# Performance work log

Measured on AMD Instinct MI355X. Metric: run time of the kernel, lower is better.

## Reference

```python
import jax, jax.numpy as jnp
from jax import lax
import numpy as np

T, B, NIN = 512, 512, 64
H1, H2, H3 = 100, 50, 25


def lstm_layer(x, w_ih, w_hh, b_ih, b_hh):
    # x: [T, B, in]; torch gate order (i, f, g, o); weights [4H, in]/[4H, H]
    H = w_hh.shape[1]
    xg = jnp.einsum('tbi,gi->tbg', x, w_ih) + b_ih + b_hh  # [T, B, 4H]

    def step(carry, xg_t):
        h, c = carry
        g = xg_t + h @ w_hh.T
        i, f, gg, o = jnp.split(g, 4, axis=-1)
        c = jax.nn.sigmoid(f) * c + jax.nn.sigmoid(i) * jnp.tanh(gg)
        h = jax.nn.sigmoid(o) * jnp.tanh(c)
        return (h, c), h

    h0 = jnp.zeros((x.shape[1], H), x.dtype)
    _, hs = lax.scan(step, (h0, h0), xg)
    return hs  # [T, B, H]


def setup_inputs() -> dict:
    key = jax.random.key(0)
    ks = jax.random.split(key, 16)
    s = 0.1  # init scale for stability
    return {
        'x': jax.random.normal(ks[0], (T, B, NIN), jnp.float32),
        'w_ih1': jax.random.normal(ks[1], (4 * H1, NIN), jnp.float32) * s,
        'w_hh1': jax.random.normal(ks[2], (4 * H1, H1), jnp.float32) * s,
        'b_ih1': jax.random.normal(ks[3], (4 * H1,), jnp.float32) * s,
        'b_hh1': jax.random.normal(ks[4], (4 * H1,), jnp.float32) * s,
        'w_ih2': jax.random.normal(ks[5], (4 * H2, H1), jnp.float32) * s,
        'w_hh2': jax.random.normal(ks[6], (4 * H2, H2), jnp.float32) * s,
        'b_ih2': jax.random.normal(ks[7], (4 * H2,), jnp.float32) * s,
        'b_hh2': jax.random.normal(ks[8], (4 * H2,), jnp.float32) * s,
        'w_ih3': jax.random.normal(ks[9], (4 * H3, H2), jnp.float32) * s,
        'w_hh3': jax.random.normal(ks[10], (4 * H3, H3), jnp.float32) * s,
        'b_ih3': jax.random.normal(ks[11], (4 * H3,), jnp.float32) * s,
        'b_hh3': jax.random.normal(ks[12], (4 * H3,), jnp.float32) * s,
        'w_lin': jax.random.normal(ks[13], (1, H3), jnp.float32) * s,
        'b_lin': jax.random.normal(ks[14], (1,), jnp.float32) * s,
    }


def reference(x, w_ih1, w_hh1, b_ih1, b_hh1,
              w_ih2, w_hh2, b_ih2, b_hh2,
              w_ih3, w_hh3, b_ih3, b_hh3,
              w_lin, b_lin):
    # Dropout layers are identity at inference.
    h = lstm_layer(x, w_ih1, w_hh1, b_ih1, b_hh1)
    h = lstm_layer(h, w_ih2, w_hh2, b_ih2, b_hh2)
    h = lstm_layer(h, w_ih3, w_hh3, b_ih3, b_hh3)
    return h @ w_lin.T + b_lin  # [T, B, 1]
```

## Files before the change

### kernel.cpp

```cpp
#include <hip/hip_runtime.h>
#include <math.h>

#define T_STEPS 512
#define BATCH   512

__device__ __forceinline__ float sigmoidf_(float x) {
    return 1.0f / (1.0f + __expf(-x));
}
__device__ __forceinline__ float tanhf_(float x) {
    float ax = fabsf(x);
    float e  = __expf(-2.0f * ax);
    float t  = (1.0f - e) / (1.0f + e);
    return copysignf(t, x);
}
__device__ __forceinline__ float4 ld4(const float* p) {
    return make_float4(p[0], p[1], p[2], p[3]);
}

__global__ __launch_bounds__(448, 2) void gemm1_kernel(
    const float* __restrict__ A, const float* __restrict__ W,
    const float* __restrict__ bih, const float* __restrict__ bhh,
    float* __restrict__ xg)
{
    __shared__ __align__(16) float As[64 * 64];
    const int tid = threadIdx.x;

    float4 W00,W01,W02,W03,W04,W05,W06,W07,W08,W09,W10,W11,W12,W13,W14,W15;
    float bias = 0.0f;
    if (tid < 400) {
        bias = bih[tid] + bhh[tid];
        const float* wp = W + tid * 64;
        W00=ld4(wp+ 0); W01=ld4(wp+ 4); W02=ld4(wp+ 8); W03=ld4(wp+12);
        W04=ld4(wp+16); W05=ld4(wp+20); W06=ld4(wp+24); W07=ld4(wp+28);
        W08=ld4(wp+32); W09=ld4(wp+36); W10=ld4(wp+40); W11=ld4(wp+44);
        W12=ld4(wp+48); W13=ld4(wp+52); W14=ld4(wp+56); W15=ld4(wp+60);
    }

    const size_t r0 = (size_t)blockIdx.x * 64;
    const float4* Ag = (const float4*)(A + r0 * 64);
    float4* As4 = (float4*)As;
    for (int i = tid; i < 64 * 16; i += 448) As4[i] = Ag[i];
    __syncthreads();

    if (tid < 400) {
        for (int r = 0; r < 64; ++r) {
            const float4* a4 = (const float4*)(As + r * 64);
            float a0 = bias, a1 = 0.0f;
#define G1V(WV, I) { float4 v = a4[I]; \
            a0 = fmaf(v.x, WV.x, a0); a1 = fmaf(v.y, WV.y, a1); \
            a0 = fmaf(v.z, WV.z, a0); a1 = fmaf(v.w, WV.w, a1); }
            G1V(W00,0) G1V(W01,1) G1V(W02,2) G1V(W03,3)
            G1V(W04,4) G1V(W05,5) G1V(W06,6) G1V(W07,7)
            G1V(W08,8) G1V(W09,9) G1V(W10,10) G1V(W11,11)
            G1V(W12,12) G1V(W13,13) G1V(W14,14) G1V(W15,15)
#undef G1V
            xg[(r0 + r) * 400 + tid] = a0 + a1;
        }
    }
}

__global__ __launch_bounds__(448, 2) void gemm2_kernel(
    const float* __restrict__ A,
    const float* __restrict__ W,
    const float* __restrict__ bih, const float* __restrict__ bhh,
    float* __restrict__ xg)
{
    __shared__ __align__(16) float As[64 * 104];
    __shared__ __align__(16) float ps[8][2][200];

    const int tid  = threadIdx.x;
    const bool slot = (tid < 400);
    const int q = slot ? tid / 200 : 0;
    const int j = slot ? tid % 200 : 0;

    float4 W00,W01,W02,W03,W04,W05,W06,W07,W08,W09,W10,W11,W12;
    float bias = 0.0f;
    if (slot) {
        if (q == 0) bias = bih[j] + bhh[j];
        const float* wp = W + j * 100 + q * 52;
        W00=ld4(wp+ 0); W01=ld4(wp+ 4); W02=ld4(wp+ 8); W03=ld4(wp+12);
        W04=ld4(wp+16); W05=ld4(wp+20); W06=ld4(wp+24); W07=ld4(wp+28);
        W08=ld4(wp+32); W09=ld4(wp+36); W10=ld4(wp+40); W11=ld4(wp+44);
        W12 = q ? make_float4(0.f,0.f,0.f,0.f) : ld4(wp+48);
    }

    const size_t r0 = (size_t)blockIdx.x * 64;
    const float2* A2 = (const float2*)(A + r0 * 100);
    float2* As2 = (float2*)As;
    for (int i = tid; i < 64 * 50; i += 448) {
        int r = i / 50, k2 = i % 50;
        As2[r * 52 + k2] = A2[i];
    }
    if (tid < 64) {
        As[tid*104+100]=0.f; As[tid*104+101]=0.f;
        As[tid*104+102]=0.f; As[tid*104+103]=0.f;
    }
    __syncthreads();

    const float4* As4 = (const float4*)As;
    const int q13 = q * 13;
    const float base = (q == 0) ? bias : 0.0f;
    for (int g = 0; g < 8; ++g) {
        const int rb = g * 8;
        if (slot) {
#define G2V(P, WV, I) { float4 v = P[I]; \
            A0 = fmaf(v.x, WV.x, A0); A1 = fmaf(v.y, WV.y, A1); \
            A0 = fmaf(v.z, WV.z, A0); A1 = fmaf(v.w, WV.w, A1); }
#define G2ROW(RR) { const float4* a4 = As4 + (rb + RR) * 26 + q13; \
            float A0 = base, A1 = 0.0f; \
            G2V(a4,W00,0) G2V(a4,W01,1) G2V(a4,W02,2) G2V(a4,W03,3) \
            G2V(a4,W04,4) G2V(a4,W05,5) G2V(a4,W06,6) G2V(a4,W07,7) \
            G2V(a4,W08,8) G2V(a4,W09,9) G2V(a4,W10,10) G2V(a4,W11,11) \
            G2V(a4,W12,12) \
            ps[RR][q][j] = A0 + A1; }
            G2ROW(0) G2ROW(1) G2ROW(2) G2ROW(3)
            G2ROW(4) G2ROW(5) G2ROW(6) G2ROW(7)
#undef G2ROW
#undef G2V
        }
        __syncthreads();
        if (tid < 200) {
            #pragma unroll
            for (int rr = 0; rr < 8; ++rr)
                xg[(r0 + rb + rr) * 200 + tid] = ps[rr][0][tid] + ps[rr][1][tid];
        }
        __syncthreads();
    }
}

__global__ __launch_bounds__(832, 3) void scan1_kernel(
    const float* __restrict__ xg,
    const float* __restrict__ w_hh,
    float* __restrict__ h1c,
    float* __restrict__ c1state,
    int t0, int CH)
{
    __shared__ __align__(16) float h_s[2][104];
    __shared__ __align__(16) float ps[2][2][400];

    const int tid   = threadIdx.x;
    const int q     = (tid >= 416) ? 1 : 0;
    const int j     = tid - 416 * q;
    const bool slot = (j < 400);
    const int brow0 = blockIdx.x * 2;

    float4 W00,W01,W02,W03,W04,W05,W06,W07,W08,W09,W10,W11,W12;
    if (slot) {
        const float* wp = w_hh + j * 100 + q * 52;
        W00=ld4(wp+ 0); W01=ld4(wp+ 4); W02=ld4(wp+ 8); W03=ld4(wp+12);
        W04=ld4(wp+16); W05=ld4(wp+20); W06=ld4(wp+24); W07=ld4(wp+28);
        W08=ld4(wp+32); W09=ld4(wp+36); W10=ld4(wp+40); W11=ld4(wp+44);
        W12 = q ? make_float4(0.f,0.f,0.f,0.f) : ld4(wp+48);
    }

    float c = 0.0f;
    if (tid < 200) {
        int bn = tid / 100, u = tid % 100;
        if (t0 == 0) {
            h_s[bn][u] = 0.0f;
        } else {
            h_s[bn][u] = h1c[((size_t)(CH - 1) * BATCH + brow0 + bn) * 100 + u];
            c          = c1state[(size_t)(brow0 + bn) * 100 + u];
        }
    }
    if (tid >= 200 && tid < 208) {
        int i = tid - 200;
        h_s[i >> 2][100 + (i & 3)] = 0.0f;
    }

    float xgv0 = 0.0f, xgv1 = 0.0f;
    if (slot && q == 0) {
        xgv0 = xg[(size_t)brow0 * 400 + j];
        xgv1 = xg[((size_t)brow0 + 1) * 400 + j];
    }
    __syncthreads();

    const int hq = q * 13;
    for (int tl = 0; tl < CH; ++tl) {
        float pre0 = 0.0f, pre1 = 0.0f;
        if (slot && q == 0 && tl + 1 < CH) {
            pre0 = xg[((size_t)(tl + 1) * BATCH + brow0) * 400 + j];
            pre1 = xg[((size_t)(tl + 1) * BATCH + brow0 + 1) * 400 + j];
        }
        if (slot) {
            const float4* h0 = (const float4*)h_s[0] + hq;
            const float4* h1 = (const float4*)h_s[1] + hq;
            float a00 = xgv0, a01 = 0.0f, a10 = xgv1, a11 = 0.0f;
#define S1ACC(WV, I) { float4 v0 = h0[I], v1 = h1[I]; \
            a00 = fmaf(v0.x, WV.x, a00); a10 = fmaf(v1.x, WV.x, a10); \
            a01 = fmaf(v0.y, WV.y, a01); a11 = fmaf(v1.y, WV.y, a11); \
            a00 = fmaf(v0.z, WV.z, a00); a10 = fmaf(v1.z, WV.z, a10); \
            a01 = fmaf(v0.w, WV.w, a01); a11 = fmaf(v1.w, WV.w, a11); }
            S1ACC(W00,0) S1ACC(W01,1) S1ACC(W02,2) S1ACC(W03,3)
            S1ACC(W04,4) S1ACC(W05,5) S1ACC(W06,6) S1ACC(W07,7)
            S1ACC(W08,8) S1ACC(W09,9) S1ACC(W10,10) S1ACC(W11,11)
            S1ACC(W12,12)
#undef S1ACC
            ps[0][q][j] = a00 + a01;
            ps[1][q][j] = a10 + a11;
        }
        __syncthreads();
        xgv0 = pre0; xgv1 = pre1;
        if (tid < 200) {
            int bn = tid / 100, u = tid % 100;
            float gi = ps[bn][0][u]       + ps[bn][1][u];
            float gf = ps[bn][0][100 + u] + ps[bn][1][100 + u];
            float gg = ps[bn][0][200 + u] + ps[bn][1][200 + u];
            float go = ps[bn][0][300 + u] + ps[bn][1][300 + u];
            c = sigmoidf_(gf) * c + sigmoidf_(gi) * tanhf_(gg);
            float h = sigmoidf_(go) * tanhf_(c);
            h_s[bn][u] = h;
            h1c[((size_t)tl * BATCH + brow0 + bn) * 100 + u] = h;
        }
        __syncthreads();
    }
    if (tid < 200) {
        int bn = tid / 100, u = tid % 100;
        c1state[(size_t)(brow0 + bn) * 100 + u] = c;
    }
}

__global__ __launch_bounds__(384, 2) void scan23_kernel(
    const float* __restrict__ xg2,
    const float* __restrict__ w_hh2,
    const float* __restrict__ w_ih3,
    const float* __restrict__ w_hh3,
    const float* __restrict__ b_ih3, const float* __restrict__ b_hh3,
    const float* __restrict__ w_lin, const float* __restrict__ b_lin,
    float* __restrict__ out,
    float* __restrict__ h2state, float* __restrict__ c2state,
    float* __restrict__ h3state, float* __restrict__ c3state,
    int t0, int CH)
{
    __shared__ __align__(16) float h2_s[52];
    __shared__ __align__(16) float x3_s[2][52];
    __shared__ __align__(16) float h3_s[28];
    __shared__ __align__(16) float h3o_s[2][28];
    __shared__ __align__(16) float g2_s[200];
    __shared__ __align__(16) float g3_s[100];

    const int tid  = threadIdx.x;
    const int brow = blockIdx.x;

    float4 WA0,WA1,WA2,WA3,WA4,WA5,WA6,WA7,WA8,WA9,WA10,WA11,WA12;
    float4 WB0,WB1,WB2,WB3,WB4,WB5,WB6;
    float bias = 0.0f;

    if (tid < 200) {
        const float* p = w_hh2 + tid * 50;
        WA0=ld4(p+ 0); WA1=ld4(p+ 4); WA2=ld4(p+ 8); WA3=ld4(p+12);
        WA4=ld4(p+16); WA5=ld4(p+20); WA6=ld4(p+24); WA7=ld4(p+28);
        WA8=ld4(p+32); WA9=ld4(p+36); WA10=ld4(p+40); WA11=ld4(p+44);
        WA12 = make_float4(p[48], p[49], 0.f, 0.f);
    } else if (tid >= 256 && tid < 356) {
        int jj = tid - 256;
        bias = b_ih3[jj] + b_hh3[jj];
        const float* p = w_ih3 + jj * 50;
        WA0=ld4(p+ 0); WA1=ld4(p+ 4); WA2=ld4(p+ 8); WA3=ld4(p+12);
        WA4=ld4(p+16); WA5=ld4(p+20); WA6=ld4(p+24); WA7=ld4(p+28);
        WA8=ld4(p+32); WA9=ld4(p+36); WA10=ld4(p+40); WA11=ld4(p+44);
        WA12 = make_float4(p[48], p[49], 0.f, 0.f);
        const float* p2 = w_hh3 + jj * 25;
        WB0=ld4(p2+ 0); WB1=ld4(p2+ 4); WB2=ld4(p2+ 8);
        WB3=ld4(p2+12); WB4=ld4(p2+16); WB5=ld4(p2+20);
        WB6 = make_float4(p2[24], 0.f, 0.f, 0.f);
    } else if (tid == 370) {
        bias = b_lin[0];
        WA0=ld4(w_lin+ 0); WA1=ld4(w_lin+ 4); WA2=ld4(w_lin+ 8);
        WA3=ld4(w_lin+12); WA4=ld4(w_lin+16); WA5=ld4(w_lin+20);
        WA6 = make_float4(w_lin[24], 0.f, 0.f, 0.f);
    }

    float c2 = 0.0f, c3 = 0.0f;
    if (tid < 52)  { h2_s[tid] = 0.0f; x3_s[0][tid] = 0.0f; x3_s[1][tid] = 0.0f; }
    if (tid >= 52 && tid < 80)  h3_s[tid - 52] = 0.0f;
    if (tid >= 80 && tid < 108) h3o_s[0][tid - 80] = 0.0f;
    if (tid >= 108 && tid < 136) h3o_s[1][tid - 108] = 0.0f;
    __syncthreads();
    if (t0 > 0) {
        if (tid < 50) {
            h2_s[tid] = h2state[(size_t)brow * 50 + tid];
            c2        = c2state[(size_t)brow * 50 + tid];
        }
        if (tid >= 256 && tid < 281) {
            int u = tid - 256;
            h3_s[u] = h3state[(size_t)brow * 25 + u];
            c3      = c3state[(size_t)brow * 25 + u];
        }
    }
    float xgv = (tid < 200) ? xg2[(size_t)brow * 200 + tid] : 0.0f;
    __syncthreads();

    for (int it = 0; it < CH + 2; ++it) {
        float pre = (tid < 200 && it + 1 < CH)
                  ? xg2[((size_t)(it + 1) * BATCH + brow) * 200 + tid] : 0.0f;

        if (tid < 200 && it < CH) {
            const float4* hv = (const float4*)h2_s;
            float a0 = xgv, a1 = 0.0f;
#define SCV(PV, WV, I) { float4 v = PV[I]; \
            a0 = fmaf(v.x, WV.x, a0); a1 = fmaf(v.y, WV.y, a1); \
            a0 = fmaf(v.z, WV.z, a0); a1 = fmaf(v.w, WV.w, a1); }
            SCV(hv,WA0,0) SCV(hv,WA1,1) SCV(hv,WA2,2) SCV(hv,WA3,3)
            SCV(hv,WA4,4) SCV(hv,WA5,5) SCV(hv,WA6,6) SCV(hv,WA7,7)
            SCV(hv,WA8,8) SCV(hv,WA9,9) SCV(hv,WA10,10) SCV(hv,WA11,11)
            SCV(hv,WA12,12)
            g2_s[tid] = a0 + a1;
        }

        if (tid >= 256 && tid < 356 && it >= 1 && it <= CH) {
            const float4* xv = (const float4*)x3_s[(it - 1) & 1];
            const float4* hv = (const float4*)h3_s;
            float a0 = bias, a1 = 0.0f;
            SCV(xv,WA0,0) SCV(xv,WA1,1) SCV(xv,WA2,2) SCV(xv,WA3,3)
            SCV(xv,WA4,4) SCV(xv,WA5,5) SCV(xv,WA6,6) SCV(xv,WA7,7)
            SCV(xv,WA8,8) SCV(xv,WA9,9) SCV(xv,WA10,10) SCV(xv,WA11,11)
            SCV(xv,WA12,12)
            SCV(hv,WB0,0) SCV(hv,WB1,1) SCV(hv,WB2,2) SCV(hv,WB3,3)
            SCV(hv,WB4,4) SCV(hv,WB5,5) SCV(hv,WB6,6)
            g3_s[tid - 256] = a0 + a1;
        }

        if (tid == 370 && it >= 2) {
            const float4* hv = (const float4*)h3o_s[(it - 2) & 1];
            float a0 = bias, a1 = 0.0f;
            SCV(hv,WA0,0) SCV(hv,WA1,1) SCV(hv,WA2,2) SCV(hv,WA3,3)
            SCV(hv,WA4,4) SCV(hv,WA5,5) SCV(hv,WA6,6)
            out[(size_t)(t0 + it - 2) * BATCH + brow] = a0 + a1;
        }
#undef SCV
        __syncthreads();

        if (tid < 200) xgv = pre;

        if (tid < 50 && it < CH) {
            float gi = g2_s[tid],       gf = g2_s[50 + tid];
            float gg = g2_s[100 + tid], go = g2_s[150 + tid];
            c2 = sigmoidf_(gf) * c2 + sigmoidf_(gi) * tanhf_(gg);
            float h = sigmoidf_(go) * tanhf_(c2);
            h2_s[tid] = h;
            x3_s[it & 1][tid] = h;
        }

        if (tid >= 256 && tid < 281 && it >= 1 && it <= CH) {
            int u = tid - 256;
            float gi = g3_s[u],      gf = g3_s[25 + u];
            float gg = g3_s[50 + u], go = g3_s[75 + u];
            c3 = sigmoidf_(gf) * c3 + sigmoidf_(gi) * tanhf_(gg);
            float h = sigmoidf_(go) * tanhf_(c3);
            h3_s[u] = h;
            h3o_s[(it - 1) & 1][u] = h;
        }
        __syncthreads();
    }

    if (tid < 50) {
        h2state[(size_t)brow * 50 + tid] = h2_s[tid];
        c2state[(size_t)brow * 50 + tid] = c2;
    }
    if (tid >= 256 && tid < 281) {
        int u = tid - 256;
        h3state[(size_t)brow * 25 + u] = h3_s[u];
        c3state[(size_t)brow * 25 + u] = c3;
    }
}

extern "C" void kernel_launch(void* const* d_in, const int* in_sizes, int n_in,
                              void* d_out, int out_size, void* d_ws, size_t ws_size,
                              hipStream_t stream)
{
    const float* x     = (const float*)d_in[0];
    const float* w_ih1 = (const float*)d_in[1];
    const float* w_hh1 = (const float*)d_in[2];
    const float* b_ih1 = (const float*)d_in[3];
    const float* b_hh1 = (const float*)d_in[4];
    const float* w_ih2 = (const float*)d_in[5];
    const float* w_hh2 = (const float*)d_in[6];
    const float* b_ih2 = (const float*)d_in[7];
    const float* b_hh2 = (const float*)d_in[8];
    const float* w_ih3 = (const float*)d_in[9];
    const float* w_hh3 = (const float*)d_in[10];
    const float* b_ih3 = (const float*)d_in[11];
    const float* b_hh3 = (const float*)d_in[12];
    const float* w_lin = (const float*)d_in[13];
    const float* b_lin = (const float*)d_in[14];
    float* out = (float*)d_out;

    const size_t state_bytes = (size_t)BATCH * (100 + 50 + 50 + 25 + 25) * sizeof(float);
    int CH = 0;
    for (int c = 128; c >= 8; c >>= 1) {
        size_t need = (size_t)c * BATCH * 700 * sizeof(float) + state_bytes;
        if (need <= ws_size) { CH = c; break; }
    }
    if (CH == 0) return;

    char* ws = (char*)d_ws;
    float* xg1c    = (float*)ws;
    float* h1c     = xg1c + (size_t)CH * BATCH * 400;
    float* xg2c    = h1c  + (size_t)CH * BATCH * 100;
    float* c1state = xg2c + (size_t)CH * BATCH * 200;
    float* h2state = c1state + (size_t)BATCH * 100;
    float* c2state = h2state + (size_t)BATCH * 50;
    float* h3state = c2state + (size_t)BATCH * 50;
    float* c3state = h3state + (size_t)BATCH * 25;

    const int rowtiles = CH * BATCH / 64;

    for (int t0 = 0; t0 < T_STEPS; t0 += CH) {
        gemm1_kernel<<<rowtiles, 448, 0, stream>>>(
            x + (size_t)t0 * BATCH * 64, w_ih1, b_ih1, b_hh1, xg1c);
        scan1_kernel<<<BATCH / 2, 832, 0, stream>>>(xg1c, w_hh1, h1c, c1state, t0, CH);
        gemm2_kernel<<<rowtiles, 448, 0, stream>>>(h1c, w_ih2, b_ih2, b_hh2, xg2c);
        scan23_kernel<<<BATCH, 384, 0, stream>>>(
            xg2c, w_hh2, w_ih3, w_hh3, b_ih3, b_hh3, w_lin, b_lin, out,
            h2state, c2state, h3state, c3state, t0, CH);
    }
}
```

Before: 1.909 ms.

## Give each thread all four gates of a hidden unit in LSTM scans

Restructures scan1 and scan23 so each thread computes all four gate pre-activations (i,f,g,o) for one hidden unit, keeping the four weight rows in registers. The nonlinearity can then run on values the thread already holds, without a shared-memory gate exchange. scan1 moves from two batch rows per 832-thread block to one row per 256-thread block. h state is double-buffered so fewer shared-memory round trips sit between the matvec and the cell update. The cost is much higher register pressure (about 52 float4 weights per thread, pinned with inline asm) and fewer active lanes per block, which risks spills or lower occupancy.

Result: slower. 5.776 ms (+202.6%).

```diff
diff --git a/kernel.cpp b/kernel.cpp
--- a/kernel.cpp
+++ b/kernel.cpp
@@ -16,6 +16,9 @@
 __device__ __forceinline__ float4 ld4(const float* p) {
     return make_float4(p[0], p[1], p[2], p[3]);
 }
+
+#define PINF(f)  asm volatile("" : "+v"(f))
+#define PIN4(v)  { PINF(v.x); PINF(v.y); PINF(v.z); PINF(v.w); }
 
 __global__ __launch_bounds__(448, 2) void gemm1_kernel(
     const float* __restrict__ A, const float* __restrict__ W,
@@ -60,8 +63,7 @@
 }
 
 __global__ __launch_bounds__(448, 2) void gemm2_kernel(
-    const float* __restrict__ A,
-    const float* __restrict__ W,
+    const float* __restrict__ A, const float* __restrict__ W,
     const float* __restrict__ bih, const float* __restrict__ bhh,
     float* __restrict__ xg)
 {
@@ -128,7 +130,7 @@
     }
 }
 
-__global__ __launch_bounds__(832, 3) void scan1_kernel(
+__global__ __launch_bounds__(256, 2) void scan1_kernel(
     const float* __restrict__ xg,
     const float* __restrict__ w_hh,
     float* __restrict__ h1c,
@@ -136,91 +138,87 @@
     int t0, int CH)
 {
     __shared__ __align__(16) float h_s[2][104];
-    __shared__ __align__(16) float ps[2][2][400];
-
-    const int tid   = threadIdx.x;
-    const int q     = (tid >= 416) ? 1 : 0;
-    const int j     = tid - 416 * q;
-    const bool slot = (j < 400);
-    const int brow0 = blockIdx.x * 2;
-
-    float4 W00,W01,W02,W03,W04,W05,W06,W07,W08,W09,W10,W11,W12;
-    if (slot) {
-        const float* wp = w_hh + j * 100 + q * 52;
-        W00=ld4(wp+ 0); W01=ld4(wp+ 4); W02=ld4(wp+ 8); W03=ld4(wp+12);
-        W04=ld4(wp+16); W05=ld4(wp+20); W06=ld4(wp+24); W07=ld4(wp+28);
-        W08=ld4(wp+32); W09=ld4(wp+36); W10=ld4(wp+40); W11=ld4(wp+44);
-        W12 = q ? make_float4(0.f,0.f,0.f,0.f) : ld4(wp+48);
-    }
-
+    __shared__ __align__(16) float ps[2][4][100];
+
+    const int tid = threadIdx.x;
+    const int row = blockIdx.x;
+    const bool act = (tid < 200);
+    const int u = act ? tid % 100 : 0;
+    const int q = act ? tid / 100 : 0;
+
+    float4 A0,A1,A2,A3,A4,A5,A6,A7,A8,A9,A10,A11,A12;
+    float4 B0,B1,B2,B3,B4,B5,B6,B7,B8,B9,B10,B11,B12;
+    float4 C0,C1,C2,C3,C4,C5,C6,C7,C8,C9,C10,C11,C12;
+    float4 D0,D1,D2,D3,D4,D5,D6,D7,D8,D9,D10,D11,D12;
+#define S1LD(P, base) \
+    P##0=ld4(base+0);  P##1=ld4(base+4);  P##2=ld4(base+8);  P##3=ld4(base+12); \
+    P##4=ld4(base+16); P##5=ld4(base+20); P##6=ld4(base+24); P##7=ld4(base+28); \
+    P##8=ld4(base+32); P##9=ld4(base+36); P##10=ld4(base+40); P##11=ld4(base+44); \
+    P##12 = q ? make_float4(0.f,0.f,0.f,0.f) : ld4(base+48); \
+    PIN4(P##0) PIN4(P##1) PIN4(P##2) PIN4(P##3) PIN4(P##4) PIN4(P##5) \
+    PIN4(P##6) PIN4(P##7) PIN4(P##8) PIN4(P##9) PIN4(P##10) PIN4(P##11) PIN4(P##12)
+    if (act) {
+        const float* wi = w_hh + (0 * 100 + u) * 100 + q * 52;
+        const float* wf = w_hh + (1 * 100 + u) * 100 + q * 52;
+        const float* wg = w_hh + (2 * 100 + u) * 100 + q * 52;
+        const float* wo = w_hh + (3 * 100 + u) * 100 + q * 52;
+        S1LD(A, wi) S1LD(B, wf) S1LD(C, wg) S1LD(D, wo)
+    }
+#undef S1LD
+
+    if (tid < 208) { int b = tid / 104, i = tid % 104; h_s[b][i] = 0.0f; }
     float c = 0.0f;
-    if (tid < 200) {
-        int bn = tid / 100, u = tid % 100;
-        if (t0 == 0) {
-            h_s[bn][u] = 0.0f;
-        } else {
-            h_s[bn][u] = h1c[((size_t)(CH - 1) * BATCH + brow0 + bn) * 100 + u];
-            c          = c1state[(size_t)(brow0 + bn) * 100 + u];
-        }
-    }
-    if (tid >= 200 && tid < 208) {
-        int i = tid - 200;
-        h_s[i >> 2][100 + (i & 3)] = 0.0f;
-    }
-
-    float xgv0 = 0.0f, xgv1 = 0.0f;
-    if (slot && q == 0) {
-        xgv0 = xg[(size_t)brow0 * 400 + j];
-        xgv1 = xg[((size_t)brow0 + 1) * 400 + j];
-    }
-    __syncthreads();
-
-    const int hq = q * 13;
+    __syncthreads();
+    if (t0 > 0 && tid < 100) {
+        h_s[0][u] = h1c[((size_t)(CH - 1) * BATCH + row) * 100 + u];
+        c         = c1state[(size_t)row * 100 + u];
+    }
+    float xgI = 0.f, xgF = 0.f, xgG = 0.f, xgO = 0.f;
+    if (tid < 100) {
+        const float* xp = xg + (size_t)row * 400 + u;
+        xgI = xp[0]; xgF = xp[100]; xgG = xp[200]; xgO = xp[300];
+    }
+    __syncthreads();
+
     for (int tl = 0; tl < CH; ++tl) {
-        float pre0 = 0.0f, pre1 = 0.0f;
-        if (slot && q == 0 && tl + 1 < CH) {
-            pre0 = xg[((size_t)(tl + 1) * BATCH + brow0) * 400 + j];
-            pre1 = xg[((size_t)(tl + 1) * BATCH + brow0 + 1) * 400 + j];
-        }
-        if (slot) {
-            const float4* h0 = (const float4*)h_s[0] + hq;
-            const float4* h1 = (const float4*)h_s[1] + hq;
-            float a00 = xgv0, a01 = 0.0f, a10 = xgv1, a11 = 0.0f;
-#define S1ACC(WV, I) { float4 v0 = h0[I], v1 = h1[I]; \
-            a00 = fmaf(v0.x, WV.x, a00); a10 = fmaf(v1.x, WV.x, a10); \
-            a01 = fmaf(v0.y, WV.y, a01); a11 = fmaf(v1.y, WV.y, a11); \
-            a00 = fmaf(v0.z, WV.z, a00); a10 = fmaf(v1.z, WV.z, a10); \
-            a01 = fmaf(v0.w, WV.w, a01); a11 = fmaf(v1.w, WV.w, a11); }
-            S1ACC(W00,0) S1ACC(W01,1) S1ACC(W02,2) S1ACC(W03,3)
-            S1ACC(W04,4) S1ACC(W05,5) S1ACC(W06,6) S1ACC(W07,7)
-            S1ACC(W08,8) S1ACC(W09,9) S1ACC(W10,10) S1ACC(W11,11)
-            S1ACC(W12,12)
-#undef S1ACC
-            ps[0][q][j] = a00 + a01;
-            ps[1][q][j] = a10 + a11;
-        }
-        __syncthreads();
-        xgv0 = pre0; xgv1 = pre1;
-        if (tid < 200) {
-            int bn = tid / 100, u = tid % 100;
-            float gi = ps[bn][0][u]       + ps[bn][1][u];
-            float gf = ps[bn][0][100 + u] + ps[bn][1][100 + u];
-            float gg = ps[bn][0][200 + u] + ps[bn][1][200 + u];
-            float go = ps[bn][0][300 + u] + ps[bn][1][300 + u];
+        float pI = 0.f, pF = 0.f, pG = 0.f, pO = 0.f;
+        if (tid < 100 && tl + 1 < CH) {
+            const float* xp = xg + ((size_t)(tl + 1) * BATCH + row) * 400 + u;
+            pI = xp[0]; pF = xp[100]; pG = xp[200]; pO = xp[300];
+        }
+        if (act) {
+            const float4* hv = (const float4*)h_s[tl & 1] + q * 13;
+            float aI = q ? 0.f : xgI, aF = q ? 0.f : xgF;
+            float aG = q ? 0.f : xgG, aO = q ? 0.f : xgO;
+#define S1F(I) { float4 v = hv[I]; \
+            aI=fmaf(v.x,A##I.x,aI); aF=fmaf(v.x,B##I.x,aF); aG=fmaf(v.x,C##I.x,aG); aO=fmaf(v.x,D##I.x,aO); \
+            aI=fmaf(v.y,A##I.y,aI); aF=fmaf(v.y,B##I.y,aF); aG=fmaf(v.y,C##I.y,aG); aO=fmaf(v.y,D##I.y,aO); \
+            aI=fmaf(v.z,A##I.z,aI); aF=fmaf(v.z,B##I.z,aF); aG=fmaf(v.z,C##I.z,aG); aO=fmaf(v.z,D##I.z,aO); \
+            aI=fmaf(v.w,A##I.w,aI); aF=fmaf(v.w,B##I.w,aF); aG=fmaf(v.w,C##I.w,aG); aO=fmaf(v.w,D##I.w,aO); }
+            S1F(0) S1F(1) S1F(2) S1F(3) S1F(4) S1F(5) S1F(6)
+            S1F(7) S1F(8) S1F(9) S1F(10) S1F(11) S1F(12)
+#undef S1F
+            ps[q][0][u] = aI; ps[q][1][u] = aF;
+            ps[q][2][u] = aG; ps[q][3][u] = aO;
+        }
+        __syncthreads();
+        xgI = pI; xgF = pF; xgG = pG; xgO = pO;
+        if (tid < 100) {
+            float gi = ps[0][0][u] + ps[1][0][u];
+            float gf = ps[0][1][u] + ps[1][1][u];
+            float gg = ps[0][2][u] + ps[1][2][u];
+            float go = ps[0][3][u] + ps[1][3][u];
             c = sigmoidf_(gf) * c + sigmoidf_(gi) * tanhf_(gg);
             float h = sigmoidf_(go) * tanhf_(c);
-            h_s[bn][u] = h;
-            h1c[((size_t)tl * BATCH + brow0 + bn) * 100 + u] = h;
-        }
-        __syncthreads();
-    }
-    if (tid < 200) {
-        int bn = tid / 100, u = tid % 100;
-        c1state[(size_t)(brow0 + bn) * 100 + u] = c;
-    }
-}
-
-__global__ __launch_bounds__(384, 2) void scan23_kernel(
+            h_s[(tl + 1) & 1][u] = h;
+            h1c[((size_t)tl * BATCH + row) * 100 + u] = h;
+        }
+        __syncthreads();
+    }
+    if (tid < 100) c1state[(size_t)row * 100 + u] = c;
+}
+
+__global__ __launch_bounds__(128, 2) void scan23_kernel(
     const float* __restrict__ xg2,
     const float* __restrict__ w_hh2,
     const float* __restrict__ w_ih3,
@@ -232,136 +230,164 @@
     float* __restrict__ h3state, float* __restrict__ c3state,
     int t0, int CH)
 {
-    __shared__ __align__(16) float h2_s[52];
+    __shared__ __align__(16) float h2_s[2][52];
     __shared__ __align__(16) float x3_s[2][52];
-    __shared__ __align__(16) float h3_s[28];
+    __shared__ __align__(16) float h3_s[2][28];
     __shared__ __align__(16) float h3o_s[2][28];
-    __shared__ __align__(16) float g2_s[200];
-    __shared__ __align__(16) float g3_s[100];
-
-    const int tid  = threadIdx.x;
-    const int brow = blockIdx.x;
-
+    __shared__ __align__(16) float ps3[2][25];
+
+    const int tid = threadIdx.x;
+    const int row = blockIdx.x;
+
+    const bool isL2 = (tid < 50);
+    const bool isL3 = (tid >= 64 && tid < 114);
+    const bool isLin = (tid == 120);
+    const int u2 = isL2 ? tid : 0;
+    const int u3 = isL3 ? (tid - 64) % 25 : 0;
+    const int p3 = isL3 ? (tid - 64) / 25 : 0;
+
+    float4 A0,A1,A2,A3,A4,A5,A6,A7,A8,A9,A10,A11,A12;
+    float4 B0,B1,B2,B3,B4,B5,B6,B7,B8,B9,B10,B11,B12;
+    float4 C0,C1,C2,C3,C4,C5,C6,C7,C8,C9,C10,C11,C12;
+    float4 D0,D1,D2,D3,D4,D5,D6,D7,D8,D9,D10,D11,D12;
     float4 WA0,WA1,WA2,WA3,WA4,WA5,WA6,WA7,WA8,WA9,WA10,WA11,WA12;
     float4 WB0,WB1,WB2,WB3,WB4,WB5,WB6;
-    float bias = 0.0f;
-
-    if (tid < 200) {
-        const float* p = w_hh2 + tid * 50;
-        WA0=ld4(p+ 0); WA1=ld4(p+ 4); WA2=ld4(p+ 8); WA3=ld4(p+12);
-        WA4=ld4(p+16); WA5=ld4(p+20); WA6=ld4(p+24); WA7=ld4(p+28);
-        WA8=ld4(p+32); WA9=ld4(p+36); WA10=ld4(p+40); WA11=ld4(p+44);
-        WA12 = make_float4(p[48], p[49], 0.f, 0.f);
-    } else if (tid >= 256 && tid < 356) {
-        int jj = tid - 256;
-        bias = b_ih3[jj] + b_hh3[jj];
-        const float* p = w_ih3 + jj * 50;
-        WA0=ld4(p+ 0); WA1=ld4(p+ 4); WA2=ld4(p+ 8); WA3=ld4(p+12);
-        WA4=ld4(p+16); WA5=ld4(p+20); WA6=ld4(p+24); WA7=ld4(p+28);
-        WA8=ld4(p+32); WA9=ld4(p+36); WA10=ld4(p+40); WA11=ld4(p+44);
-        WA12 = make_float4(p[48], p[49], 0.f, 0.f);
-        const float* p2 = w_hh3 + jj * 25;
-        WB0=ld4(p2+ 0); WB1=ld4(p2+ 4); WB2=ld4(p2+ 8);
-        WB3=ld4(p2+12); WB4=ld4(p2+16); WB5=ld4(p2+20);
-        WB6 = make_float4(p2[24], 0.f, 0.f, 0.f);
-    } else if (tid == 370) {
-        bias = b_lin[0];
-        WA0=ld4(w_lin+ 0); WA1=ld4(w_lin+ 4); WA2=ld4(w_lin+ 8);
-        WA3=ld4(w_lin+12); WA4=ld4(w_lin+16); WA5=ld4(w_lin+20);
-        WA6 = make_float4(w_lin[24], 0.f, 0.f, 0.f);
-    }
-
-    float c2 = 0.0f, c3 = 0.0f;
-    if (tid < 52)  { h2_s[tid] = 0.0f; x3_s[0][tid] = 0.0f; x3_s[1][tid] = 0.0f; }
-    if (tid >= 52 && tid < 80)  h3_s[tid - 52] = 0.0f;
-    if (tid >= 80 && tid < 108) h3o_s[0][tid - 80] = 0.0f;
-    if (tid >= 108 && tid < 136) h3o_s[1][tid - 108] = 0.0f;
+    float4 WC0,WC1,WC2,WC3,WC4,WC5,WC6,WC7,WC8,WC9,WC10,WC11,WC12;
+    float4 WD0,WD1,WD2,WD3,WD4,WD5,WD6;
+    float biasA = 0.f, biasB = 0.f;
+
+#define LD50(P, base) \
+    P##0=ld4(base+0);  P##1=ld4(base+4);  P##2=ld4(base+8);  P##3=ld4(base+12); \
+    P##4=ld4(base+16); P##5=ld4(base+20); P##6=ld4(base+24); P##7=ld4(base+28); \
+    P##8=ld4(base+32); P##9=ld4(base+36); P##10=ld4(base+40); P##11=ld4(base+44); \
+    P##12 = make_float4(base[48], base[49], 0.f, 0.f);
+#define LD25(P, base) \
+    P##0=ld4(base+0);  P##1=ld4(base+4);  P##2=ld4(base+8); \
+    P##3=ld4(base+12); P##4=ld4(base+16); P##5=ld4(base+20); \
+    P##6 = make_float4(base[24], 0.f, 0.f, 0.f);
+
+    if (isL2) {
+        LD50(A, (w_hh2 + (0 * 50 + u2) * 50))
+        LD50(B, (w_hh2 + (1 * 50 + u2) * 50))
+        LD50(C, (w_hh2 + (2 * 50 + u2) * 50))
+        LD50(D, (w_hh2 + (3 * 50 + u2) * 50))
+    } else if (isL3) {
+        const int ja = (2 * p3)     * 25 + u3;
+        const int jb = (2 * p3 + 1) * 25 + u3;
+        biasA = b_ih3[ja] + b_hh3[ja];
+        biasB = b_ih3[jb] + b_hh3[jb];
+        LD50(WA, (w_ih3 + ja * 50))
+        LD25(WB, (w_hh3 + ja * 25))
+        LD50(WC, (w_ih3 + jb * 50))
+        LD25(WD, (w_hh3 + jb * 25))
+    } else if (isLin) {
+        biasA = b_lin[0];
+        LD25(WB, w_lin)
+    }
+#undef LD50
+#undef LD25
+
+    if (tid < 104) { int b = tid / 52, i = tid % 52; h2_s[b][i] = 0.f; x3_s[b][i] = 0.f; }
+    if (tid >= 104 && tid < 128) { int k = tid - 104; int b = k / 12, i = k % 12;
+        if (i < 28) {  } h3_s[b][i] = 0.f; h3o_s[b][i] = 0.f; }
+    if (tid < 2) { for (int i = 12; i < 28; ++i) { h3_s[tid][i] = 0.f; h3o_s[tid][i] = 0.f; } }
+    float c2 = 0.f, c3 = 0.f;
     __syncthreads();
     if (t0 > 0) {
-        if (tid < 50) {
-            h2_s[tid] = h2state[(size_t)brow * 50 + tid];
-            c2        = c2state[(size_t)brow * 50 + tid];
-        }
-        if (tid >= 256 && tid < 281) {
-            int u = tid - 256;
-            h3_s[u] = h3state[(size_t)brow * 25 + u];
-            c3      = c3state[(size_t)brow * 25 + u];
-        }
-    }
-    float xgv = (tid < 200) ? xg2[(size_t)brow * 200 + tid] : 0.0f;
+        if (isL2) {
+            h2_s[0][u2] = h2state[(size_t)row * 50 + u2];
+            c2          = c2state[(size_t)row * 50 + u2];
+        }
+        if (isL3 && p3 == 0) {
+            h3_s[0][u3] = h3state[(size_t)row * 25 + u3];
+            c3          = c3state[(size_t)row * 25 + u3];
+        }
+    }
+    float xI = 0.f, xF = 0.f, xG = 0.f, xO = 0.f;
+    if (isL2) {
+        const float* xp = xg2 + (size_t)row * 200 + u2;
+        xI = xp[0]; xF = xp[50]; xG = xp[100]; xO = xp[150];
+    }
     __syncthreads();
 
     for (int it = 0; it < CH + 2; ++it) {
-        float pre = (tid < 200 && it + 1 < CH)
-                  ? xg2[((size_t)(it + 1) * BATCH + brow) * 200 + tid] : 0.0f;
-
-        if (tid < 200 && it < CH) {
-            const float4* hv = (const float4*)h2_s;
-            float a0 = xgv, a1 = 0.0f;
-#define SCV(PV, WV, I) { float4 v = PV[I]; \
-            a0 = fmaf(v.x, WV.x, a0); a1 = fmaf(v.y, WV.y, a1); \
-            a0 = fmaf(v.z, WV.z, a0); a1 = fmaf(v.w, WV.w, a1); }
-            SCV(hv,WA0,0) SCV(hv,WA1,1) SCV(hv,WA2,2) SCV(hv,WA3,3)
-            SCV(hv,WA4,4) SCV(hv,WA5,5) SCV(hv,WA6,6) SCV(hv,WA7,7)
-            SCV(hv,WA8,8) SCV(hv,WA9,9) SCV(hv,WA10,10) SCV(hv,WA11,11)
-            SCV(hv,WA12,12)
-            g2_s[tid] = a0 + a1;
-        }
-
-        if (tid >= 256 && tid < 356 && it >= 1 && it <= CH) {
-            const float4* xv = (const float4*)x3_s[(it - 1) & 1];
-            const float4* hv = (const float4*)h3_s;
-            float a0 = bias, a1 = 0.0f;
-            SCV(xv,WA0,0) SCV(xv,WA1,1) SCV(xv,WA2,2) SCV(xv,WA3,3)
-            SCV(xv,WA4,4) SCV(xv,WA5,5) SCV(xv,WA6,6) SCV(xv,WA7,7)
-            SCV(xv,WA8,8) SCV(xv,WA9,9) SCV(xv,WA10,10) SCV(xv,WA11,11)
-            SCV(xv,WA12,12)
-            SCV(hv,WB0,0) SCV(hv,WB1,1) SCV(hv,WB2,2) SCV(hv,WB3,3)
-            SCV(hv,WB4,4) SCV(hv,WB5,5) SCV(hv,WB6,6)
-            g3_s[tid - 256] = a0 + a1;
-        }
-
-        if (tid == 370 && it >= 2) {
+        float pI = 0.f, pF = 0.f, pG = 0.f, pO = 0.f;
+        if (isL2 && it + 1 < CH) {
+            const float* xp = xg2 + ((size_t)(it + 1) * BATCH + row) * 200 + u2;
+            pI = xp[0]; pF = xp[50]; pG = xp[100]; pO = xp[150];
+        }
+        float aI = 0.f, aF = 0.f, aG = 0.f, aO = 0.f;
+        float aA = biasA, aB = biasB;
+        if (isL2 && it < CH) {
+            const float4* hv = (const float4*)h2_s[it & 1];
+            aI = xI; aF = xF; aG = xG; aO = xO;
+#define L2F(I) { float4 v = hv[I]; \
+            aI=fmaf(v.x,A##I.x,aI); aF=fmaf(v.x,B##I.x,aF); aG=fmaf(v.x,C##I.x,aG); aO=fmaf(v.x,D##I.x,aO); \
+            aI=fmaf(v.y,A##I.y,aI); aF=fmaf(v.y,B##I.y,aF); aG=fmaf(v.y,C##I.y,aG); aO=fmaf(v.y,D##I.y,aO); \
+            aI=fmaf(v.z,A##I.z,aI); aF=fmaf(v.z,B##I.z,aF); aG=fmaf(v.z,C##I.z,aG); aO=fmaf(v.z,D##I.z,aO); \
+            aI=fmaf(v.w,A##I.w,aI); aF=fmaf(v.w,B##I.w,aF); aG=fmaf(v.w,C##I.w,aG); aO=fmaf(v.w,D##I.w,aO); }
+            L2F(0) L2F(1) L2F(2) L2F(3) L2F(4) L2F(5) L2F(6)
+            L2F(7) L2F(8) L2F(9) L2F(10) L2F(11) L2F(12)
+#undef L2F
+        }
+        if (isL3 && it >= 1 && it <= CH) {
+            const int s3 = it - 1;
+            const float4* xv = (const float4*)x3_s[s3 & 1];
+            const float4* hv = (const float4*)h3_s[s3 & 1];
+#define L3X(I) { float4 v = xv[I]; \
+            aA=fmaf(v.x,WA##I.x,aA); aB=fmaf(v.x,WC##I.x,aB); \
+            aA=fmaf(v.y,WA##I.y,aA); aB=fmaf(v.y,WC##I.y,aB); \
+            aA=fmaf(v.z,WA##I.z,aA); aB=fmaf(v.z,WC##I.z,aB); \
+            aA=fmaf(v.w,WA##I.w,aA); aB=fmaf(v.w,WC##I.w,aB); }
+#define L3H(I) { float4 v = hv[I]; \
+            aA=fmaf(v.x,WB##I.x,aA); aB=fmaf(v.x,WD##I.x,aB); \
+            aA=fmaf(v.y,WB##I.y,aA); aB=fmaf(v.y,WD##I.y,aB); \
+            aA=fmaf(v.z,WB##I.z,aA); aB=fmaf(v.z,WD##I.z,aB); \
+            aA=fmaf(v.w,WB##I.w,aA); aB=fmaf(v.w,WD##I.w,aB); }
+            L3X(0) L3X(1) L3X(2) L3X(3) L3X(4) L3X(5) L3X(6)
+            L3X(7) L3X(8) L3X(9) L3X(10) L3X(11) L3X(12)
+            L3H(0) L3H(1) L3H(2) L3H(3) L3H(4) L3H(5) L3H(6)
+#undef L3X
+#undef L3H
+            if (p3 == 1) { ps3[0][u3] = aA; ps3[1][u3] = aB; }
+        }
+        if (isLin && it >= 2) {
             const float4* hv = (const float4*)h3o_s[(it - 2) & 1];
-            float a0 = bias, a1 = 0.0f;
-            SCV(hv,WA0,0) SCV(hv,WA1,1) SCV(hv,WA2,2) SCV(hv,WA3,3)
-            SCV(hv,WA4,4) SCV(hv,WA5,5) SCV(hv,WA6,6)
-            out[(size_t)(t0 + it - 2) * BATCH + brow] = a0 + a1;
-        }
-#undef SCV
-        __syncthreads();
-
-        if (tid < 200) xgv = pre;
-
-        if (tid < 50 && it < CH) {
-            float gi = g2_s[tid],       gf = g2_s[50 + tid];
-            float gg = g2_s[100 + tid], go = g2_s[150 + tid];
-            c2 = sigmoidf_(gf) * c2 + sigmoidf_(gi) * tanhf_(gg);
-            float h = sigmoidf_(go) * tanhf_(c2);
-            h2_s[tid] = h;
-            x3_s[it & 1][tid] = h;
-        }
-
-        if (tid >= 256 && tid < 281 && it >= 1 && it <= CH) {
-            int u = tid - 256;
-            float gi = g3_s[u],      gf = g3_s[25 + u];
-            float gg = g3_s[50 + u], go = g3_s[75 + u];
-            c3 = sigmoidf_(gf) * c3 + sigmoidf_(gi) * tanhf_(gg);
+            float o0 = biasA, o1 = 0.f;
+#define LNF(I) { float4 v = hv[I]; \
+            o0 = fmaf(v.x, WB##I.x, o0); o1 = fmaf(v.y, WB##I.y, o1); \
+            o0 = fmaf(v.z, WB##I.z, o0); o1 = fmaf(v.w, WB##I.w, o1); }
+            LNF(0) LNF(1) LNF(2) LNF(3) LNF(4) LNF(5) LNF(6)
+#undef LNF
+            out[(size_t)(t0 + it - 2) * BATCH + row] = o0 + o1;
+        }
+        __syncthreads();
+
+        if (isL2) { xI = pI; xF = pF; xG = pG; xO = pO; }
+        if (isL2 && it < CH) {
+            c2 = sigmoidf_(aF) * c2 + sigmoidf_(aI) * tanhf_(aG);
+            float h = sigmoidf_(aO) * tanhf_(c2);
+            h2_s[(it + 1) & 1][u2] = h;
+            x3_s[it & 1][u2] = h;
+        }
+        if (isL3 && p3 == 0 && it >= 1 && it <= CH) {
+            const int s3 = it - 1;
+            float gg = ps3[0][u3], go = ps3[1][u3];
+            c3 = sigmoidf_(aB) * c3 + sigmoidf_(aA) * tanhf_(gg);
             float h = sigmoidf_(go) * tanhf_(c3);
-            h3_s[u] = h;
-            h3o_s[(it - 1) & 1][u] = h;
-        }
-        __syncthreads();
-    }
-
-    if (tid < 50) {
-        h2state[(size_t)brow * 50 + tid] = h2_s[tid];
-        c2state[(size_t)brow * 50 + tid] = c2;
-    }
-    if (tid >= 256 && tid < 281) {
-        int u = tid - 256;
-        h3state[(size_t)brow * 25 + u] = h3_s[u];
-        c3state[(size_t)brow * 25 + u] = c3;
+            h3_s[(s3 + 1) & 1][u3] = h;
+            h3o_s[s3 & 1][u3] = h;
+        }
+        __syncthreads();
+    }
+
+    if (isL2) {
+        h2state[(size_t)row * 50 + u2] = h2_s[CH & 1][u2];
+        c2state[(size_t)row * 50 + u2] = c2;
+    }
+    if (isL3 && p3 == 0) {
+        h3state[(size_t)row * 25 + u3] = h3_s[CH & 1][u3];
+        c3state[(size_t)row * 25 + u3] = c3;
     }
 }
 
@@ -409,9 +435,9 @@
     for (int t0 = 0; t0 < T_STEPS; t0 += CH) {
         gemm1_kernel<<<rowtiles, 448, 0, stream>>>(
             x + (size_t)t0 * BATCH * 64, w_ih1, b_ih1, b_hh1, xg1c);
-        scan1_kernel<<<BATCH / 2, 832, 0, stream>>>(xg1c, w_hh1, h1c, c1state, t0, CH);
+        scan1_kernel<<<BATCH, 256, 0, stream>>>(xg1c, w_hh1, h1c, c1state, t0, CH);
         gemm2_kernel<<<rowtiles, 448, 0, stream>>>(h1c, w_ih2, b_ih2, b_hh2, xg2c);
-        scan23_kernel<<<BATCH, 384, 0, stream>>>(
+        scan23_kernel<<<BATCH, 128, 0, stream>>>(
             xg2c, w_hh2, w_ih3, w_hh3, b_ih3, b_hh3, w_lin, b_lin, out,
             h2state, c2state, h3state, c3state, t0, CH);
     }
```
